# Kernel optimization log

Measured on AMD Instinct MI355X. Metric: run time of the kernel, lower is better.

## Reference

```python
import jax, jax.numpy as jnp
import numpy as np

B, H, W = 8, 56, 56
DIM, DIM_OUT, NUM_HEADS = 96, 192, 3
Q_STRIDE = (2, 2)


def setup_inputs() -> dict:
    key = jax.random.key(0)
    k1, k2, k3 = jax.random.split(key, 3)
    x = jax.random.normal(k1, (B, H, W, DIM), dtype=jnp.float32)
    W_qkv = jax.random.normal(k2, (DIM, 3 * DIM_OUT), dtype=jnp.float32) * 0.02
    b_qkv = jnp.zeros((3 * DIM_OUT,), dtype=jnp.float32)
    W_proj = jax.random.normal(k3, (DIM_OUT, DIM_OUT), dtype=jnp.float32) * 0.02
    b_proj = jnp.zeros((DIM_OUT,), dtype=jnp.float32)
    return {"x": x, "W_qkv": W_qkv, "b_qkv": b_qkv, "W_proj": W_proj, "b_proj": b_proj}


def reference(x, W_qkv, b_qkv, W_proj, b_proj):
    b, h, w, _ = x.shape
    c = W_proj.shape[0]          # dim_out
    nh = NUM_HEADS
    hd = c // nh                 # head_dim
    sh, sw = Q_STRIDE

    # fused QKV projection: (B,H,W,3*C)
    qkv = jnp.einsum("bhwd,de->bhwe", x, W_qkv) + b_qkv
    qkv = qkv.reshape(b, h * w, 3, nh, hd)
    q, k, v = qkv[:, :, 0], qkv[:, :, 1], qkv[:, :, 2]  # each (B,N,nh,hd)

    # query max-pool over spatial dims (channels = nh*hd, heads interleaved as in original)
    q = q.reshape(b, h, w, c)
    q = q.reshape(b, h // sh, sh, w // sw, sw, c).max(axis=(2, 4))  # (B,H',W',C)
    hn, wn = h // sh, w // sw
    q = q.reshape(b, hn * wn, nh, hd)

    # heads-first layout, scaled q
    q = q.transpose(0, 2, 1, 3) / jnp.sqrt(jnp.asarray(hd, x.dtype))  # (B,nh,Nq,hd)
    k = k.transpose(0, 2, 1, 3)                                       # (B,nh,Nk,hd)
    v = v.transpose(0, 2, 1, 3)

    attn = jax.nn.softmax(jnp.einsum("bnqd,bnkd->bnqk", q, k), axis=-1)
    out = jnp.einsum("bnqk,bnkd->bnqd", attn, v)        # (B,nh,Nq,hd)
    out = out.transpose(0, 2, 1, 3).reshape(b, hn, wn, c)

    return jnp.einsum("bhwc,cd->bhwd", out, W_proj) + b_proj
```

## Files before the change

### kernel.cpp

```cpp
#include <hip/hip_runtime.h>

#define BB    8
#define E3    576
#define DIMO  192
#define NH    3
#define HD    64
#define NK    3136
#define NQ    784
#define M1    25088
#define M2    6272
#define KSPLIT 7
#define KSLICE 448
#define PSTR  56

typedef __bf16 bf16x8 __attribute__((ext_vector_type(8)));
typedef float f32x4  __attribute__((ext_vector_type(4)));

__device__ inline unsigned short f2bf(float f) {
    unsigned int u = __builtin_bit_cast(unsigned int, f);
    u += 0x7FFFu + ((u >> 16) & 1u);
    return (unsigned short)(u >> 16);
}

__global__ void wprep(const float* __restrict__ Wqkv, const float* __restrict__ Wproj,
                      unsigned short* __restrict__ Wb, unsigned short* __restrict__ Wpb) {
    __shared__ float Ls[192][33];
    const int t = threadIdx.x;
    if (blockIdx.x < 18) {
        const int n0 = blockIdx.x * 32;
        int rr = t >> 5, c = t & 31;
#pragma unroll
        for (int rb = 0; rb < 12; ++rb) {
            int row = rb * 8 + rr;
            Ls[row][c] = Wqkv[(size_t)row * 576 + n0 + c];
        }
        __syncthreads();
        int n = t >> 3, kc = (t & 7) * 12;
#pragma unroll
        for (int j = 0; j < 12; j += 4) {
            ushort4 u = { f2bf(Ls[kc + j][n]), f2bf(Ls[kc + j + 1][n]),
                          f2bf(Ls[kc + j + 2][n]), f2bf(Ls[kc + j + 3][n]) };
            *(ushort4*)(Wb + (size_t)(n0 + n) * 96 + kc + j) = u;
        }
    } else {
        const int n0 = (blockIdx.x - 18) * 32;
        int rr = t >> 5, c = t & 31;
#pragma unroll
        for (int rb = 0; rb < 24; ++rb) {
            int row = rb * 8 + rr;
            Ls[row][c] = Wproj[(size_t)row * 192 + n0 + c];
        }
        __syncthreads();
        int n = t >> 3, kc = (t & 7) * 24;
#pragma unroll
        for (int j = 0; j < 24; j += 4) {
            ushort4 u = { f2bf(Ls[kc + j][n]), f2bf(Ls[kc + j + 1][n]),
                          f2bf(Ls[kc + j + 2][n]), f2bf(Ls[kc + j + 3][n]) };
            *(ushort4*)(Wpb + (size_t)(n0 + n) * 192 + kc + j) = u;
        }
    }
}

__launch_bounds__(256)
__global__ void qkv_mfma(const float* __restrict__ x,
                         const unsigned short* __restrict__ Wb,
                         const float* __restrict__ bias,
                         float* __restrict__ Qtmp,
                         unsigned short* __restrict__ Kb,
                         unsigned short* __restrict__ Vt) {
    __shared__ __attribute__((aligned(16))) unsigned short xs[64 * 104];
    const int tid = threadIdx.x;
    const int wave = tid >> 6, lane = tid & 63;
    const int quad = lane >> 4, l16 = lane & 15;
    const int ntile = blockIdx.x;
    const int m0 = blockIdx.y * 64;

#pragma unroll
    for (int i = 0; i < 6; ++i) {
        int f = tid + i * 256;
        int r = f / 24, c4 = f % 24;
        float4 v = ((const float4*)x)[(size_t)(m0 + r) * 24 + c4];
        ushort4 u = { f2bf(v.x), f2bf(v.y), f2bf(v.z), f2bf(v.w) };
        *(ushort4*)&xs[r * 104 + c4 * 4] = u;
    }
    __syncthreads();

    f32x4 acc[12];
#pragma unroll
    for (int i = 0; i < 12; ++i) acc[i] = (f32x4){0.f, 0.f, 0.f, 0.f};

    const unsigned short* wb = Wb + (size_t)(ntile * 192 + l16) * 96 + quad * 8;
#pragma unroll
    for (int ch = 0; ch < 3; ++ch) {
        bf16x8 af = *(const bf16x8*)&xs[(wave * 16 + l16) * 104 + ch * 32 + quad * 8];
#pragma unroll
        for (int nf = 0; nf < 12; ++nf) {
            bf16x8 bfr = *(const bf16x8*)(wb + (size_t)nf * 16 * 96 + ch * 32);
            acc[nf] = __builtin_amdgcn_mfma_f32_16x16x32_bf16(af, bfr, acc[nf], 0, 0, 0);
        }
    }

    const int mbase = m0 + wave * 16 + quad * 4;
    if (ntile == 0) {
#pragma unroll
        for (int nf = 0; nf < 12; ++nf) {
            int n = nf * 16 + l16;
            float bs = bias[n];
#pragma unroll
            for (int i = 0; i < 4; ++i)
                Qtmp[(size_t)(mbase + i) * 192 + n] = acc[nf][i] + bs;
        }
    } else if (ntile == 1) {
#pragma unroll
        for (int nf = 0; nf < 12; ++nf) {
            int n = nf * 16 + l16;
            float bs = bias[192 + n];
#pragma unroll
            for (int i = 0; i < 4; ++i)
                Kb[(size_t)(mbase + i) * 192 + n] = f2bf(acc[nf][i] + bs);
        }
    } else {
        int b = m0 / NK;
        int key = mbase - b * NK;
#pragma unroll
        for (int nf = 0; nf < 12; ++nf) {
            int n = nf * 16 + l16;
            float bs = bias[384 + n];
            int hh = n >> 6, dd = n & 63;
            ushort4 u = { f2bf(acc[nf][0] + bs), f2bf(acc[nf][1] + bs),
                          f2bf(acc[nf][2] + bs), f2bf(acc[nf][3] + bs) };
            *(ushort4*)(Vt + ((size_t)((b * 3 + hh) * 64 + dd)) * NK + key) = u;
        }
    }
}

__global__ void qpool_bf16(const float* __restrict__ Qtmp, unsigned short* __restrict__ Qpb) {
    int idx = blockIdx.x * 256 + threadIdx.x;
    int d  = idx & 63;
    int q  = (idx >> 6) % NQ;
    int bh = idx / (64 * NQ);
    int b = bh / NH, h = bh % NH;
    int hq = q / 28, wq = q % 28;
    const float* base = Qtmp + (size_t)b * NK * 192 + h * 64 + d;
    int r0 = (2 * hq) * 56 + 2 * wq;
    float m = base[(size_t)r0 * 192];
    m = fmaxf(m, base[(size_t)(r0 + 1) * 192]);
    m = fmaxf(m, base[(size_t)(r0 + 56) * 192]);
    m = fmaxf(m, base[(size_t)(r0 + 57) * 192]);
    Qpb[idx] = f2bf(m * 0.125f);
}

__launch_bounds__(256)
__global__ void attn_mfma(const unsigned short* __restrict__ Qpb,
                          const unsigned short* __restrict__ Kb,
                          const unsigned short* __restrict__ Vt,
                          float* __restrict__ Pnum,
                          float* __restrict__ Pden) {
    __shared__ __attribute__((aligned(16))) unsigned short Ks[64 * 88];
    __shared__ __attribute__((aligned(16))) unsigned short Vs[64 * 88];
    __shared__ __attribute__((aligned(16))) unsigned short Ps[4 * 32 * PSTR];

    const int tid = threadIdx.x;
    const int wave = tid >> 6, lane = tid & 63;
    const int quad = lane >> 4, l16 = lane & 15;
    const int bh = blockIdx.y, b = bh / NH, h = bh % NH;
    const int qt = blockIdx.x * 128 + wave * 32;
    const int ks = blockIdx.z, k00 = ks * KSLICE;

    const int srow0 = tid >> 3, sch = (tid & 7) * 8;
    const unsigned short* kg  = Kb + ((size_t)(b * NK + k00) + srow0) * DIMO + h * 64 + sch;
    const unsigned short* kg1 = kg + (size_t)32 * DIMO;
    const unsigned short* vg  = Vt + ((size_t)bh * 64 + srow0) * NK + k00 + sch;
    const unsigned short* vg1 = vg + (size_t)32 * NK;

    uint4 kp0 = *(const uint4*)kg;
    uint4 kp1 = *(const uint4*)kg1;
    uint4 vp0 = *(const uint4*)vg;
    uint4 vp1 = *(const uint4*)vg1;

    int qa = min(qt + l16, NQ - 1);
    int qb = min(qt + 16 + l16, NQ - 1);
    const unsigned short* qpa = Qpb + ((size_t)bh * NQ + qa) * HD + quad * 8;
    const unsigned short* qpc = Qpb + ((size_t)bh * NQ + qb) * HD + quad * 8;
    bf16x8 qf[2][2];
    qf[0][0] = *(const bf16x8*)qpa;  qf[0][1] = *(const bf16x8*)(qpa + 32);
    qf[1][0] = *(const bf16x8*)qpc;  qf[1][1] = *(const bf16x8*)(qpc + 32);

    f32x4 on[4][2];
#pragma unroll
    for (int i = 0; i < 4; ++i)
#pragma unroll
        for (int j = 0; j < 2; ++j) on[i][j] = (f32x4){0.f, 0.f, 0.f, 0.f};
    float dden0 = 0.f, dden1 = 0.f;

    unsigned short* myP = Ps + wave * 32 * PSTR;

    for (int s = 0; s < 7; ++s) {
        __syncthreads();
        *(uint4*)&Ks[srow0 * 88 + sch]        = kp0;
        *(uint4*)&Ks[(srow0 + 32) * 88 + sch] = kp1;
        *(uint4*)&Vs[srow0 * 88 + sch]        = vp0;
        *(uint4*)&Vs[(srow0 + 32) * 88 + sch] = vp1;
        __syncthreads();
        if (s < 6) {
            kp0 = *(const uint4*)(kg  + (size_t)(s + 1) * 64 * DIMO);
            kp1 = *(const uint4*)(kg1 + (size_t)(s + 1) * 64 * DIMO);
            vp0 = *(const uint4*)(vg  + (s + 1) * 64);
            vp1 = *(const uint4*)(vg1 + (s + 1) * 64);
        }

#pragma unroll
        for (int half = 0; half < 2; ++half) {
#pragma unroll
            for (int ksub = 0; ksub < 2; ++ksub) {
                const int krow = (half * 32 + ksub * 16 + l16) * 88;
                bf16x8 kf0 = *(const bf16x8*)&Ks[krow + quad * 8];
                bf16x8 kf1 = *(const bf16x8*)&Ks[krow + 32 + quad * 8];
#pragma unroll
                for (int qsub = 0; qsub < 2; ++qsub) {
                    f32x4 sa = (f32x4){0.f, 0.f, 0.f, 0.f};
                    sa = __builtin_amdgcn_mfma_f32_16x16x32_bf16(kf0, qf[qsub][0], sa, 0, 0, 0);
                    sa = __builtin_amdgcn_mfma_f32_16x16x32_bf16(kf1, qf[qsub][1], sa, 0, 0, 0);
                    float p0 = __expf(sa[0]), p1 = __expf(sa[1]);
                    float p2 = __expf(sa[2]), p3 = __expf(sa[3]);
                    if (qsub == 0) dden0 += (p0 + p1) + (p2 + p3);
                    else           dden1 += (p0 + p1) + (p2 + p3);
                    ushort4 pw = { f2bf(p0), f2bf(p1), f2bf(p2), f2bf(p3) };
                    *(ushort4*)&myP[(qsub * 16 + l16) * PSTR + ksub * 16 + quad * 4] = pw;
                }
            }
            bf16x8 pf0 = *(const bf16x8*)&myP[l16 * PSTR + quad * 8];
            bf16x8 pf1 = *(const bf16x8*)&myP[(16 + l16) * PSTR + quad * 8];
#pragma unroll
            for (int dsub = 0; dsub < 4; ++dsub) {
                bf16x8 vf = *(const bf16x8*)&Vs[(dsub * 16 + l16) * 88 + half * 32 + quad * 8];
                on[dsub][0] = __builtin_amdgcn_mfma_f32_16x16x32_bf16(vf, pf0, on[dsub][0], 0, 0, 0);
                on[dsub][1] = __builtin_amdgcn_mfma_f32_16x16x32_bf16(vf, pf1, on[dsub][1], 0, 0, 0);
            }
        }
    }

#pragma unroll
    for (int qsub = 0; qsub < 2; ++qsub) {
        float r = (qsub == 0) ? dden0 : dden1;
        r += __shfl_xor(r, 16, 64);
        r += __shfl_xor(r, 32, 64);
        int q = qt + qsub * 16 + l16;
        if (q < NQ) {
            size_t base = (size_t)ks * (24 * NQ * HD) + ((size_t)bh * NQ + q) * HD + quad * 4;
#pragma unroll
            for (int dsub = 0; dsub < 4; ++dsub)
                *(f32x4*)(Pnum + base + dsub * 16) = on[dsub][qsub];
            if (quad == 0) Pden[ks * (24 * NQ) + bh * NQ + q] = r;
        }
    }
}

__global__ void combine_kernel(const float* __restrict__ Pnum,
                               const float* __restrict__ Pden,
                               unsigned short* __restrict__ AObf) {
    int idx = blockIdx.x * 256 + threadIdx.x;
    int d = idx & 63;
    int rest = idx >> 6;
    int qq = rest % NQ;
    int bh = rest / NQ;
    int b = bh / NH, h = bh % NH;
    float num = 0.f, den = 0.f;
#pragma unroll
    for (int s = 0; s < KSPLIT; ++s) {
        num += Pnum[(size_t)s * (24 * NQ * HD) + idx];
        den += Pden[s * (24 * NQ) + bh * NQ + qq];
    }
    AObf[((size_t)b * NQ + qq) * DIMO + h * 64 + d] = f2bf(num / den);
}

__launch_bounds__(256)
__global__ void proj_mfma(const unsigned short* __restrict__ AObf,
                          const unsigned short* __restrict__ Wpb,
                          const float* __restrict__ bproj,
                          float* __restrict__ out) {
    __shared__ __attribute__((aligned(16))) unsigned short as_[64 * 200];
    const int tid = threadIdx.x;
    const int wave = tid >> 6, lane = tid & 63;
    const int quad = lane >> 4, l16 = lane & 15;
    const int ntile = blockIdx.x;
    const int m0 = blockIdx.y * 64;

#pragma unroll
    for (int i = 0; i < 6; ++i) {
        int f = tid + i * 256;
        int r = f / 24, c = f % 24;
        *(uint4*)&as_[r * 200 + c * 8] = *(const uint4*)(AObf + (size_t)(m0 + r) * 192 + c * 8);
    }
    __syncthreads();

    f32x4 acc[4];
#pragma unroll
    for (int i = 0; i < 4; ++i) acc[i] = (f32x4){0.f, 0.f, 0.f, 0.f};

    const unsigned short* wp = Wpb + (size_t)(ntile * 64 + l16) * 192 + quad * 8;
#pragma unroll
    for (int ch = 0; ch < 6; ++ch) {
        bf16x8 af = *(const bf16x8*)&as_[(wave * 16 + l16) * 200 + ch * 32 + quad * 8];
#pragma unroll
        for (int nf = 0; nf < 4; ++nf) {
            bf16x8 bfr = *(const bf16x8*)(wp + (size_t)nf * 16 * 192 + ch * 32);
            acc[nf] = __builtin_amdgcn_mfma_f32_16x16x32_bf16(af, bfr, acc[nf], 0, 0, 0);
        }
    }

    const int m = m0 + wave * 16 + quad * 4;
#pragma unroll
    for (int nf = 0; nf < 4; ++nf) {
        int n = ntile * 64 + nf * 16 + l16;
        float bs = bproj[n];
#pragma unroll
        for (int i = 0; i < 4; ++i)
            out[(size_t)(m + i) * 192 + n] = acc[nf][i] + bs;
    }
}

extern "C" void kernel_launch(void* const* d_in, const int* in_sizes, int n_in,
                              void* d_out, int out_size, void* d_ws, size_t ws_size,
                              hipStream_t stream) {
    const float* x     = (const float*)d_in[0];
    const float* Wqkv  = (const float*)d_in[1];
    const float* bqkv  = (const float*)d_in[2];
    const float* Wproj = (const float*)d_in[3];
    const float* bproj = (const float*)d_in[4];
    float* out = (float*)d_out;

    float* Qtmp = (float*)d_ws;
    float* Pnum = Qtmp + (size_t)M1 * 192;
    float* Pden = Pnum + (size_t)KSPLIT * 24 * NQ * HD;
    unsigned short* AObf = (unsigned short*)(Pden + (size_t)KSPLIT * 24 * NQ);
    unsigned short* Qpb = AObf + (size_t)M2 * DIMO;
    unsigned short* Kb  = Qpb + (size_t)24 * NQ * HD;
    unsigned short* Vt  = Kb + (size_t)BB * NK * DIMO;
    unsigned short* Wb  = Vt + (size_t)24 * HD * NK;
    unsigned short* Wpb = Wb + (size_t)576 * 96;

    wprep<<<24, 256, 0, stream>>>(Wqkv, Wproj, Wb, Wpb);

    qkv_mfma<<<dim3(3, M1 / 64), 256, 0, stream>>>(x, Wb, bqkv, Qtmp, Kb, Vt);

    qpool_bf16<<<(24 * NQ * HD) / 256, 256, 0, stream>>>(Qtmp, Qpb);

    attn_mfma<<<dim3(7, 24, KSPLIT), 256, 0, stream>>>(Qpb, Kb, Vt, Pnum, Pden);

    combine_kernel<<<(24 * NQ * HD) / 256, 256, 0, stream>>>(Pnum, Pden, AObf);

    proj_mfma<<<dim3(3, M2 / 64), 256, 0, stream>>>(AObf, Wpb, bproj, out);
}
```

Baseline: 145.9 us.

## Fuse query max-pool into QKV GEMM and split-K combine into projection

The Q section of the QKV GEMM now runs in dedicated blocks. Each loads two image rows of x, permutes them in shared memory so every 2x2 pooling window falls inside one MFMA accumulator fragment, and writes the pooled, scaled bf16 Q directly. This removes the fp32 Qtmp buffer and the separate pooling kernel. The split-K combine is folded into the projection kernel, which sums Pnum/Pden into shared memory before the GEMM, removing the AObf round trip and a launch. The projection grid shrinks to 98 blocks that each cover all 192 output columns, which may leave the GPU underoccupied.

Result: faster. 134.3 us (-7.9%).

```diff
diff --git a/kernel.cpp b/kernel.cpp
--- a/kernel.cpp
+++ b/kernel.cpp
@@ -1,7 +1,6 @@
 #include <hip/hip_runtime.h>
 
 #define BB    8
-#define E3    576
 #define DIMO  192
 #define NH    3
 #define HD    64
@@ -62,92 +61,122 @@
 }
 
 __launch_bounds__(256)
-__global__ void qkv_mfma(const float* __restrict__ x,
-                         const unsigned short* __restrict__ Wb,
-                         const float* __restrict__ bias,
-                         float* __restrict__ Qtmp,
-                         unsigned short* __restrict__ Kb,
-                         unsigned short* __restrict__ Vt) {
-    __shared__ __attribute__((aligned(16))) unsigned short xs[64 * 104];
+__global__ void qkv_fused(const float* __restrict__ x,
+                          const unsigned short* __restrict__ Wb,
+                          const float* __restrict__ bias,
+                          unsigned short* __restrict__ Qpb,
+                          unsigned short* __restrict__ Kb,
+                          unsigned short* __restrict__ Vt) {
+    __shared__ __attribute__((aligned(16))) unsigned short xs[112 * 104];
     const int tid = threadIdx.x;
     const int wave = tid >> 6, lane = tid & 63;
     const int quad = lane >> 4, l16 = lane & 15;
-    const int ntile = blockIdx.x;
-    const int m0 = blockIdx.y * 64;
-
-#pragma unroll
-    for (int i = 0; i < 6; ++i) {
-        int f = tid + i * 256;
-        int r = f / 24, c4 = f % 24;
-        float4 v = ((const float4*)x)[(size_t)(m0 + r) * 24 + c4];
-        ushort4 u = { f2bf(v.x), f2bf(v.y), f2bf(v.z), f2bf(v.w) };
-        *(ushort4*)&xs[r * 104 + c4 * 4] = u;
-    }
-    __syncthreads();
-
-    f32x4 acc[12];
-#pragma unroll
-    for (int i = 0; i < 12; ++i) acc[i] = (f32x4){0.f, 0.f, 0.f, 0.f};
-
-    const unsigned short* wb = Wb + (size_t)(ntile * 192 + l16) * 96 + quad * 8;
-#pragma unroll
-    for (int ch = 0; ch < 3; ++ch) {
-        bf16x8 af = *(const bf16x8*)&xs[(wave * 16 + l16) * 104 + ch * 32 + quad * 8];
-#pragma unroll
-        for (int nf = 0; nf < 12; ++nf) {
-            bf16x8 bfr = *(const bf16x8*)(wb + (size_t)nf * 16 * 96 + ch * 32);
-            acc[nf] = __builtin_amdgcn_mfma_f32_16x16x32_bf16(af, bfr, acc[nf], 0, 0, 0);
-        }
-    }
-
-    const int mbase = m0 + wave * 16 + quad * 4;
-    if (ntile == 0) {
-#pragma unroll
-        for (int nf = 0; nf < 12; ++nf) {
-            int n = nf * 16 + l16;
-            float bs = bias[n];
-#pragma unroll
-            for (int i = 0; i < 4; ++i)
-                Qtmp[(size_t)(mbase + i) * 192 + n] = acc[nf][i] + bs;
-        }
-    } else if (ntile == 1) {
-#pragma unroll
-        for (int nf = 0; nf < 12; ++nf) {
-            int n = nf * 16 + l16;
-            float bs = bias[192 + n];
-#pragma unroll
-            for (int i = 0; i < 4; ++i)
-                Kb[(size_t)(mbase + i) * 192 + n] = f2bf(acc[nf][i] + bs);
+    const int bid = blockIdx.x;
+
+    if (bid < 784) {
+        const int sec = (bid < 392) ? 1 : 2;
+        const int m0 = ((bid < 392) ? bid : bid - 392) * 64;
+#pragma unroll
+        for (int i = 0; i < 6; ++i) {
+            int f = tid + i * 256;
+            int r = f / 24, c4 = f % 24;
+            float4 v = ((const float4*)x)[(size_t)(m0 + r) * 24 + c4];
+            ushort4 u = { f2bf(v.x), f2bf(v.y), f2bf(v.z), f2bf(v.w) };
+            *(ushort4*)&xs[r * 104 + c4 * 4] = u;
+        }
+        __syncthreads();
+
+        f32x4 acc[12];
+#pragma unroll
+        for (int i = 0; i < 12; ++i) acc[i] = (f32x4){0.f, 0.f, 0.f, 0.f};
+
+        const unsigned short* wb = Wb + (size_t)(sec * 192 + l16) * 96 + quad * 8;
+#pragma unroll
+        for (int ch = 0; ch < 3; ++ch) {
+            bf16x8 af = *(const bf16x8*)&xs[(wave * 16 + l16) * 104 + ch * 32 + quad * 8];
+#pragma unroll
+            for (int nf = 0; nf < 12; ++nf) {
+                bf16x8 bfr = *(const bf16x8*)(wb + (size_t)nf * 16 * 96 + ch * 32);
+                acc[nf] = __builtin_amdgcn_mfma_f32_16x16x32_bf16(af, bfr, acc[nf], 0, 0, 0);
+            }
+        }
+
+        const int mbase = m0 + wave * 16 + quad * 4;
+        if (sec == 1) {
+#pragma unroll
+            for (int nf = 0; nf < 12; ++nf) {
+                int n = nf * 16 + l16;
+                float bs = bias[192 + n];
+#pragma unroll
+                for (int i = 0; i < 4; ++i)
+                    Kb[(size_t)(mbase + i) * 192 + n] = f2bf(acc[nf][i] + bs);
+            }
+        } else {
+            int b = m0 / NK;
+            int key = mbase - b * NK;
+#pragma unroll
+            for (int nf = 0; nf < 12; ++nf) {
+                int n = nf * 16 + l16;
+                float bs = bias[384 + n];
+                int hh = n >> 6, dd = n & 63;
+                ushort4 u = { f2bf(acc[nf][0] + bs), f2bf(acc[nf][1] + bs),
+                              f2bf(acc[nf][2] + bs), f2bf(acc[nf][3] + bs) };
+                *(ushort4*)(Vt + ((size_t)((b * 3 + hh) * 64 + dd)) * NK + key) = u;
+            }
         }
     } else {
-        int b = m0 / NK;
-        int key = mbase - b * NK;
-#pragma unroll
-        for (int nf = 0; nf < 12; ++nf) {
-            int n = nf * 16 + l16;
-            float bs = bias[384 + n];
-            int hh = n >> 6, dd = n & 63;
-            ushort4 u = { f2bf(acc[nf][0] + bs), f2bf(acc[nf][1] + bs),
-                          f2bf(acc[nf][2] + bs), f2bf(acc[nf][3] + bs) };
-            *(ushort4*)(Vt + ((size_t)((b * 3 + hh) * 64 + dd)) * NK + key) = u;
-        }
-    }
-}
-
-__global__ void qpool_bf16(const float* __restrict__ Qtmp, unsigned short* __restrict__ Qpb) {
-    int idx = blockIdx.x * 256 + threadIdx.x;
-    int d  = idx & 63;
-    int q  = (idx >> 6) % NQ;
-    int bh = idx / (64 * NQ);
-    int b = bh / NH, h = bh % NH;
-    int hq = q / 28, wq = q % 28;
-    const float* base = Qtmp + (size_t)b * NK * 192 + h * 64 + d;
-    int r0 = (2 * hq) * 56 + 2 * wq;
-    float m = base[(size_t)r0 * 192];
-    m = fmaxf(m, base[(size_t)(r0 + 1) * 192]);
-    m = fmaxf(m, base[(size_t)(r0 + 56) * 192]);
-    m = fmaxf(m, base[(size_t)(r0 + 57) * 192]);
-    Qpb[idx] = f2bf(m * 0.125f);
+        const int t = bid - 784;
+        const int b = t / 28, hq = t % 28;
+        const int m0 = b * NK + hq * 112;
+#pragma unroll
+        for (int i = 0; i < 11; ++i) {
+            int f = tid + i * 256;
+            if (f < 2688) {
+                int r = f / 24, c4 = f % 24;
+                float4 v = ((const float4*)x)[(size_t)(m0 + r) * 24 + c4];
+                int rp = 2 * (r % 56) + (r / 56);
+                ushort4 u = { f2bf(v.x), f2bf(v.y), f2bf(v.z), f2bf(v.w) };
+                *(ushort4*)&xs[rp * 104 + c4 * 4] = u;
+            }
+        }
+        __syncthreads();
+
+        f32x4 acc[7][3];
+#pragma unroll
+        for (int i = 0; i < 7; ++i)
+#pragma unroll
+            for (int j = 0; j < 3; ++j) acc[i][j] = (f32x4){0.f, 0.f, 0.f, 0.f};
+
+        const unsigned short* wb = Wb + (size_t)(wave * 48 + l16) * 96 + quad * 8;
+#pragma unroll
+        for (int ch = 0; ch < 3; ++ch) {
+            bf16x8 bfr[3];
+#pragma unroll
+            for (int jf = 0; jf < 3; ++jf)
+                bfr[jf] = *(const bf16x8*)(wb + (size_t)jf * 16 * 96 + ch * 32);
+#pragma unroll
+            for (int mf = 0; mf < 7; ++mf) {
+                bf16x8 a = *(const bf16x8*)&xs[(mf * 16 + l16) * 104 + ch * 32 + quad * 8];
+#pragma unroll
+                for (int jf = 0; jf < 3; ++jf)
+                    acc[mf][jf] = __builtin_amdgcn_mfma_f32_16x16x32_bf16(a, bfr[jf], acc[mf][jf], 0, 0, 0);
+            }
+        }
+
+#pragma unroll
+        for (int mf = 0; mf < 7; ++mf) {
+            int q = hq * 28 + mf * 4 + quad;
+#pragma unroll
+            for (int jf = 0; jf < 3; ++jf) {
+                int n = wave * 48 + jf * 16 + l16;
+                float m = fmaxf(fmaxf(acc[mf][jf][0], acc[mf][jf][1]),
+                                fmaxf(acc[mf][jf][2], acc[mf][jf][3]));
+                m = (m + bias[n]) * 0.125f;
+                int hh = n >> 6, dd = n & 63;
+                Qpb[((size_t)(b * 3 + hh) * NQ + q) * 64 + dd] = f2bf(m);
+            }
+        }
+    }
 }
 
 __launch_bounds__(256)
@@ -256,67 +285,83 @@
     }
 }
 
-__global__ void combine_kernel(const float* __restrict__ Pnum,
-                               const float* __restrict__ Pden,
-                               unsigned short* __restrict__ AObf) {
-    int idx = blockIdx.x * 256 + threadIdx.x;
-    int d = idx & 63;
-    int rest = idx >> 6;
-    int qq = rest % NQ;
-    int bh = rest / NQ;
-    int b = bh / NH, h = bh % NH;
-    float num = 0.f, den = 0.f;
-#pragma unroll
-    for (int s = 0; s < KSPLIT; ++s) {
-        num += Pnum[(size_t)s * (24 * NQ * HD) + idx];
-        den += Pden[s * (24 * NQ) + bh * NQ + qq];
-    }
-    AObf[((size_t)b * NQ + qq) * DIMO + h * 64 + d] = f2bf(num / den);
-}
-
 __launch_bounds__(256)
-__global__ void proj_mfma(const unsigned short* __restrict__ AObf,
+__global__ void proj_comb(const float* __restrict__ Pnum,
+                          const float* __restrict__ Pden,
                           const unsigned short* __restrict__ Wpb,
                           const float* __restrict__ bproj,
                           float* __restrict__ out) {
     __shared__ __attribute__((aligned(16))) unsigned short as_[64 * 200];
+    __shared__ float rden[64][4];
     const int tid = threadIdx.x;
     const int wave = tid >> 6, lane = tid & 63;
     const int quad = lane >> 4, l16 = lane & 15;
-    const int ntile = blockIdx.x;
-    const int m0 = blockIdx.y * 64;
-
-#pragma unroll
-    for (int i = 0; i < 6; ++i) {
-        int f = tid + i * 256;
-        int r = f / 24, c = f % 24;
-        *(uint4*)&as_[r * 200 + c * 8] = *(const uint4*)(AObf + (size_t)(m0 + r) * 192 + c * 8);
+    const int m0 = blockIdx.x * 64;
+
+    if (tid < 192) {
+        int r = tid / 3, h = tid % 3;
+        int gq = m0 + r, b = gq / NQ, qq = gq - b * NQ;
+        float den = 0.f;
+#pragma unroll
+        for (int s = 0; s < KSPLIT; ++s)
+            den += Pden[s * (24 * NQ) + (b * 3 + h) * NQ + qq];
+        rden[r][h] = 1.0f / den;
     }
     __syncthreads();
 
-    f32x4 acc[4];
-#pragma unroll
-    for (int i = 0; i < 4; ++i) acc[i] = (f32x4){0.f, 0.f, 0.f, 0.f};
-
-    const unsigned short* wp = Wpb + (size_t)(ntile * 64 + l16) * 192 + quad * 8;
+    {
+        int r = tid >> 2, cl = tid & 3;
+        int gq = m0 + r, b = gq / NQ, qq = gq - b * NQ;
+#pragma unroll
+        for (int i = 0; i < 12; ++i) {
+            int c = cl + i * 4;
+            int h = c >> 4, d = (c & 15) * 4;
+            const float* p = Pnum + ((size_t)(b * 3 + h) * NQ + qq) * 64 + d;
+            f32x4 num = (f32x4){0.f, 0.f, 0.f, 0.f};
+#pragma unroll
+            for (int s = 0; s < KSPLIT; ++s)
+                num = num + *(const f32x4*)(p + (size_t)s * (24 * NQ * HD));
+            float rc = rden[r][h];
+            ushort4 u = { f2bf(num[0] * rc), f2bf(num[1] * rc),
+                          f2bf(num[2] * rc), f2bf(num[3] * rc) };
+            *(ushort4*)&as_[r * 200 + c * 4] = u;
+        }
+    }
+    __syncthreads();
+
+    f32x4 acc[4][3];
+#pragma unroll
+    for (int i = 0; i < 4; ++i)
+#pragma unroll
+        for (int j = 0; j < 3; ++j) acc[i][j] = (f32x4){0.f, 0.f, 0.f, 0.f};
+
+    const unsigned short* wp = Wpb + (size_t)(wave * 48 + l16) * 192 + quad * 8;
 #pragma unroll
     for (int ch = 0; ch < 6; ++ch) {
-        bf16x8 af = *(const bf16x8*)&as_[(wave * 16 + l16) * 200 + ch * 32 + quad * 8];
-#pragma unroll
-        for (int nf = 0; nf < 4; ++nf) {
-            bf16x8 bfr = *(const bf16x8*)(wp + (size_t)nf * 16 * 192 + ch * 32);
-            acc[nf] = __builtin_amdgcn_mfma_f32_16x16x32_bf16(af, bfr, acc[nf], 0, 0, 0);
-        }
-    }
-
-    const int m = m0 + wave * 16 + quad * 4;
-#pragma unroll
-    for (int nf = 0; nf < 4; ++nf) {
-        int n = ntile * 64 + nf * 16 + l16;
-        float bs = bproj[n];
-#pragma unroll
-        for (int i = 0; i < 4; ++i)
-            out[(size_t)(m + i) * 192 + n] = acc[nf][i] + bs;
+        bf16x8 bfr[3];
+#pragma unroll
+        for (int jf = 0; jf < 3; ++jf)
+            bfr[jf] = *(const bf16x8*)(wp + (size_t)jf * 16 * 192 + ch * 32);
+#pragma unroll
+        for (int mf = 0; mf < 4; ++mf) {
+            bf16x8 a = *(const bf16x8*)&as_[(mf * 16 + l16) * 200 + ch * 32 + quad * 8];
+#pragma unroll
+            for (int jf = 0; jf < 3; ++jf)
+                acc[mf][jf] = __builtin_amdgcn_mfma_f32_16x16x32_bf16(a, bfr[jf], acc[mf][jf], 0, 0, 0);
+        }
+    }
+
+#pragma unroll
+    for (int mf = 0; mf < 4; ++mf) {
+        int m = m0 + mf * 16 + quad * 4;
+#pragma unroll
+        for (int jf = 0; jf < 3; ++jf) {
+            int n = wave * 48 + jf * 16 + l16;
+            float bs = bproj[n];
+#pragma unroll
+            for (int i = 0; i < 4; ++i)
+                out[(size_t)(m + i) * 192 + n] = acc[mf][jf][i] + bs;
+        }
     }
 }
 
@@ -330,11 +375,9 @@
     const float* bproj = (const float*)d_in[4];
     float* out = (float*)d_out;
 
-    float* Qtmp = (float*)d_ws;
-    float* Pnum = Qtmp + (size_t)M1 * 192;
+    float* Pnum = (float*)d_ws;
     float* Pden = Pnum + (size_t)KSPLIT * 24 * NQ * HD;
-    unsigned short* AObf = (unsigned short*)(Pden + (size_t)KSPLIT * 24 * NQ);
-    unsigned short* Qpb = AObf + (size_t)M2 * DIMO;
+    unsigned short* Qpb = (unsigned short*)(Pden + (size_t)KSPLIT * 24 * NQ);
     unsigned short* Kb  = Qpb + (size_t)24 * NQ * HD;
     unsigned short* Vt  = Kb + (size_t)BB * NK * DIMO;
     unsigned short* Wb  = Vt + (size_t)24 * HD * NK;
@@ -342,13 +385,9 @@
 
     wprep<<<24, 256, 0, stream>>>(Wqkv, Wproj, Wb, Wpb);
 
-    qkv_mfma<<<dim3(3, M1 / 64), 256, 0, stream>>>(x, Wb, bqkv, Qtmp, Kb, Vt);
-
-    qpool_bf16<<<(24 * NQ * HD) / 256, 256, 0, stream>>>(Qtmp, Qpb);
+    qkv_fused<<<1008, 256, 0, stream>>>(x, Wb, bqkv, Qpb, Kb, Vt);
 
     attn_mfma<<<dim3(7, 24, KSPLIT), 256, 0, stream>>>(Qpb, Kb, Vt, Pnum, Pden);
 
-    combine_kernel<<<(24 * NQ * HD) / 256, 256, 0, stream>>>(Pnum, Pden, AObf);
-
-    proj_mfma<<<dim3(3, M2 / 64), 256, 0, stream>>>(AObf, Wpb, bproj, out);
-}
+    proj_comb<<<98, 256, 0, stream>>>(Pnum, Pden, Wpb, bproj, out);
+}
```
